# Kernel tuning notes

Measured on AMD Instinct MI355X. Metric: run time of the kernel, lower is better.

## Reference

```python
import jax, jax.numpy as jnp
import numpy as np

T, B, M, H = 2048, 16, 512, 256
R_MIN, R_MAX, MAX_PHASE = 0.0, 1.0, 6.28


def setup_inputs() -> dict:
    key = jax.random.key(0)
    ks = jax.random.split(key, 10)
    inputs = jax.random.normal(ks[0], (T, B, M), dtype=jnp.float32)
    h_re = jnp.zeros((B, H), dtype=jnp.float32)
    h_im = jnp.zeros((B, H), dtype=jnp.float32)
    # parameter inits matching the torch module (stable |lambda| < 1)
    u1 = jax.random.uniform(ks[1], (H,), dtype=jnp.float32)
    nu_log = jnp.log(-0.5 * jnp.log(u1 * (R_MAX**2 - R_MIN**2) + R_MIN**2))
    u2 = jax.random.uniform(ks[2], (H,), dtype=jnp.float32)
    theta_log = jnp.log(MAX_PHASE * u2)
    lam = jnp.exp(-jnp.exp(nu_log) + 1j * jnp.exp(theta_log))
    gamma_log = jnp.log(jnp.sqrt(1.0 - jnp.abs(lam) ** 2))
    B_re = jax.random.normal(ks[3], (H, M), dtype=jnp.float32) / np.sqrt(2 * M)
    B_im = jax.random.normal(ks[4], (H, M), dtype=jnp.float32) / np.sqrt(2 * M)
    C_re = jax.random.normal(ks[5], (M, H), dtype=jnp.float32) / np.sqrt(H)
    C_im = jax.random.normal(ks[6], (M, H), dtype=jnp.float32) / np.sqrt(H)
    D = jax.random.normal(ks[7], (M,), dtype=jnp.float32)
    return {"inputs": inputs, "h_re": h_re, "h_im": h_im,
            "nu_log": nu_log, "theta_log": theta_log, "gamma_log": gamma_log,
            "B_re": B_re, "B_im": B_im, "C_re": C_re, "C_im": C_im, "D": D}


def reference(inputs, h_re, h_im, nu_log, theta_log, gamma_log,
              B_re, B_im, C_re, C_im, D):
    # diag_lambda = exp(-exp(nu) + i exp(theta)), shape [H]
    lam = jnp.exp(jnp.complex64(-jnp.exp(nu_log) + 1j * jnp.exp(theta_log)))
    B_norm = (B_re + 1j * B_im) * jnp.exp(gamma_log)[:, None]  # [H, M] complex
    C = C_re + 1j * C_im                                        # [M, H] complex
    h0 = (h_re + 1j * h_im).astype(jnp.complex64)               # [B, H]
    Bu = inputs.astype(jnp.complex64) @ B_norm.T                # [T, B, H] precomputed input drive

    def step(h, xs):
        bu_t, x_t = xs
        h = h * lam + bu_t                                      # [B, H]
        y = jnp.real(h @ C.T) + D * x_t                         # [B, M]
        return h, y

    h_final, outputs = jax.lax.scan(step, h0, (Bu, inputs))
    return outputs, h_final
```

## Files before the change

### kernel.cpp

```cpp
#include <hip/hip_runtime.h>
#include <hip/hip_bf16.h>
#include <math.h>

#define T_DIM 2048
#define B_DIM 16
#define M_DIM 512
#define H_DIM 256
#define KC 512
#define K_DIM 512
#define CHUNK 64
#define NCHUNK 32
#define BK 32
#define NT (K_DIM / BK)

typedef unsigned short ushort_t;
typedef __attribute__((ext_vector_type(8))) short short8;
typedef __attribute__((ext_vector_type(8))) unsigned short ushort8;
typedef __attribute__((ext_vector_type(4))) float f32x4;

#define WS_LAM   0
#define WS_LAML  512
#define WS_CARRY 1024
#define WS_WB_BF 263168
#define WS_WC_BF 394240
#define WS_BU    525312

__device__ inline ushort_t f2bf(float f) {
    __hip_bfloat16 h = __float2bfloat16(f);
    return *reinterpret_cast<ushort_t*>(&h);
}
__device__ inline float bf2f(ushort_t u) {
    union { unsigned int i; float f; } v;
    v.i = ((unsigned int)u) << 16;
    return v.f;
}

__global__ void prep_lam(const float* __restrict__ nu_log,
                         const float* __restrict__ theta_log,
                         float* __restrict__ ws) {
    int h = threadIdx.x;
    float nu = expf(nu_log[h]);
    float th = expf(theta_log[h]);
    float r  = expf(-nu);
    ws[WS_LAM + h]        = r * cosf(th);
    ws[WS_LAM + 256 + h]  = r * sinf(th);
    float rL  = expf(-64.f * nu);
    float thL = 64.f * th;
    ws[WS_LAML + h]       = rL * cosf(thL);
    ws[WS_LAML + 256 + h] = rL * sinf(thL);
}

__global__ void prep_w(const float* __restrict__ B_re, const float* __restrict__ B_im,
                       const float* __restrict__ gamma_log,
                       const float* __restrict__ C_re, const float* __restrict__ C_im,
                       ushort_t* __restrict__ wb, ushort_t* __restrict__ wc) {
    int idx = blockIdx.x * blockDim.x + threadIdx.x;
    int e    = idx & 7;
    int slot = (idx >> 3) & 511;
    int row  = slot & 127;
    int ks   = slot >> 7;
    int t    = (idx >> 12) & 15;
    int blk  = idx >> 16;
    int j = blk * 128 + row;
    int k = t * 32 + ks * 8 + e;
    float v;
    if (j < 256) v = expf(gamma_log[j])       * B_re[j * 512 + k];
    else         v = expf(gamma_log[j - 256]) * B_im[(j - 256) * 512 + k];
    wb[idx] = f2bf(v);
    float w;
    if (k < 256) w =  C_re[j * 256 + k];
    else         w = -C_im[j * 256 + (k - 256)];
    wc[idx] = f2bf(w);
}

template <int A_BF16, int OUT_BF16>
__global__ __launch_bounds__(256) void gemm_mfma(
    const void* __restrict__ Aptr, const ushort_t* __restrict__ Wt,
    void* __restrict__ Cv, const float* __restrict__ Dv,
    const float* __restrict__ X) {
    __shared__ ushort_t Asl[2][4096];
    __shared__ ushort_t Bsl[2][4096];
    const int tid = threadIdx.x;
    const int bm = blockIdx.x << 7;
    const int bnb = blockIdx.y;
    const int bn = bnb << 7;
    const int lane = tid & 63;
    const int wid  = tid >> 6;
    const int wr  = (wid >> 1) << 6;
    const int wcc = (wid & 1) << 6;
    const int l16 = lane & 15;
    const int ksl = lane >> 4;

    const int c0 = tid, c1 = tid + 256;
    const int arow = tid >> 1;
    const int aks  = (tid & 1) << 1;
    const int as0  = (aks * 128 + arow) * 8;
    const int as1  = as0 + 1024;

    const float*    Af = (const float*)Aptr;
    const ushort_t* Ab = (const ushort_t*)Aptr;

    f32x4 acc[4][4] = {};
    float4 pva0, pva1, pvb0, pvb1;
    ushort8 pua0, pua1;

    auto stageB = [&](int t, int buf) {
        size_t base = ((size_t)(bnb * NT + t)) * 4096;
        __builtin_amdgcn_global_load_lds(
            (const __attribute__((address_space(1))) void*)(Wt + base + c0 * 8),
            (__attribute__((address_space(3))) void*)(&Bsl[buf][c0 * 8]), 16, 0, 0);
        __builtin_amdgcn_global_load_lds(
            (const __attribute__((address_space(1))) void*)(Wt + base + c1 * 8),
            (__attribute__((address_space(3))) void*)(&Bsl[buf][c1 * 8]), 16, 0, 0);
    };
    auto loadA = [&](int t) {
        if constexpr (A_BF16) {
            const ushort_t* p = Ab + (size_t)(bm + arow) * K_DIM + t * BK + aks * 8;
            pua0 = *(const ushort8*)(p);
            pua1 = *(const ushort8*)(p + 8);
        } else {
            const float* p = Af + (size_t)(bm + arow) * K_DIM + t * BK + aks * 8;
            pva0 = *(const float4*)(p);
            pva1 = *(const float4*)(p + 4);
            pvb0 = *(const float4*)(p + 8);
            pvb1 = *(const float4*)(p + 12);
        }
    };
    auto writeA = [&](int buf) {
        ushort8 u0, u1;
        if constexpr (A_BF16) {
            u0 = pua0; u1 = pua1;
        } else {
            u0[0] = f2bf(pva0.x); u0[1] = f2bf(pva0.y); u0[2] = f2bf(pva0.z); u0[3] = f2bf(pva0.w);
            u0[4] = f2bf(pva1.x); u0[5] = f2bf(pva1.y); u0[6] = f2bf(pva1.z); u0[7] = f2bf(pva1.w);
            u1[0] = f2bf(pvb0.x); u1[1] = f2bf(pvb0.y); u1[2] = f2bf(pvb0.z); u1[3] = f2bf(pvb0.w);
            u1[4] = f2bf(pvb1.x); u1[5] = f2bf(pvb1.y); u1[6] = f2bf(pvb1.z); u1[7] = f2bf(pvb1.w);
        }
        *(ushort8*)(&Asl[buf][as0]) = u0;
        *(ushort8*)(&Asl[buf][as1]) = u1;
    };

    stageB(0, 0);
    loadA(0);
    writeA(0);
    __syncthreads();

    int cur = 0;
#pragma unroll 2
    for (int t = 0; t < NT; ++t) {
        const int nxt = cur ^ 1;
        if (t + 1 < NT) { stageB(t + 1, nxt); loadA(t + 1); }
        short8 afr[4], bfr[4];
#pragma unroll
        for (int m = 0; m < 4; ++m)
            afr[m] = *(const short8*)(&Asl[cur][(ksl * 128 + wr + m * 16 + l16) * 8]);
#pragma unroll
        for (int n = 0; n < 4; ++n)
            bfr[n] = *(const short8*)(&Bsl[cur][(ksl * 128 + wcc + n * 16 + l16) * 8]);
#pragma unroll
        for (int m = 0; m < 4; ++m)
#pragma unroll
            for (int n = 0; n < 4; ++n)
                acc[m][n] = __builtin_amdgcn_mfma_f32_16x16x32_bf16(
                    afr[m], bfr[n], acc[m][n], 0, 0, 0);
        if (t + 1 < NT) writeA(nxt);
        __syncthreads();
        cur = nxt;
    }

    const int fr = (lane >> 4) << 2;
#pragma unroll
    for (int m = 0; m < 4; ++m) {
#pragma unroll
        for (int n = 0; n < 4; ++n) {
#pragma unroll
            for (int r = 0; r < 4; ++r) {
                int row = bm + wr + m * 16 + fr + r;
                int col = bn + wcc + n * 16 + l16;
                size_t o = (size_t)row * 512 + col;
                float v = acc[m][n][r];
                if constexpr (OUT_BF16) {
                    ((ushort_t*)Cv)[o] = f2bf(v);
                } else {
                    ((float*)Cv)[o] = v + Dv[col] * X[o];
                }
            }
        }
    }
}

__global__ __launch_bounds__(256) void scan_local(float* __restrict__ ws) {
    const int c = blockIdx.x >> 4;
    const int b = blockIdx.x & 15;
    const int h = threadIdx.x;
    const float lr = ws[WS_LAM + h], li = ws[WS_LAM + 256 + h];
    const ushort_t* Bu = (const ushort_t*)(ws + WS_BU);
    float hr = 0.f, hi = 0.f;
    const int t0 = c * CHUNK;
    for (int l = 0; l < CHUNK; ++l) {
        size_t idx = ((size_t)(t0 + l) * B_DIM + b) * KC + h;
        float br = bf2f(Bu[idx]), bi = bf2f(Bu[idx + 256]);
        float nr = fmaf(lr, hr, fmaf(-li, hi, br));
        float ni = fmaf(lr, hi, fmaf(li, hr, bi));
        hr = nr; hi = ni;
    }
    size_t cidx = ((size_t)(c * B_DIM + b)) * KC + h;
    ws[WS_CARRY + cidx]       = hr;
    ws[WS_CARRY + cidx + 256] = hi;
}

__global__ __launch_bounds__(256) void scan_carry(float* __restrict__ ws,
        const float* __restrict__ h_re, const float* __restrict__ h_im,
        float* __restrict__ out, int out_size) {
    const int b = blockIdx.x;
    const int h = threadIdx.x;
    const float Lr = ws[WS_LAML + h], Li = ws[WS_LAML + 256 + h];
    float cr = h_re[b * H_DIM + h], ci = h_im[b * H_DIM + h];
    for (int c = 0; c < NCHUNK; ++c) {
        size_t cidx = ((size_t)(c * B_DIM + b)) * KC + h;
        float sr = ws[WS_CARRY + cidx], si = ws[WS_CARRY + cidx + 256];
        ws[WS_CARRY + cidx]       = cr;
        ws[WS_CARRY + cidx + 256] = ci;
        float nr = fmaf(Lr, cr, fmaf(-Li, ci, sr));
        float ni = fmaf(Lr, ci, fmaf(Li, cr, si));
        cr = nr; ci = ni;
    }
    const size_t base = (size_t)T_DIM * B_DIM * M_DIM;
    const size_t idx  = (size_t)b * H_DIM + h;
    size_t ore = base + idx;
    size_t oim = base + (size_t)B_DIM * H_DIM + idx;
    if (ore < (size_t)out_size) out[ore] = cr;
    if (oim < (size_t)out_size) out[oim] = ci;
}

__global__ __launch_bounds__(256) void scan_apply(float* __restrict__ ws) {
    const int c = blockIdx.x >> 4;
    const int b = blockIdx.x & 15;
    const int h = threadIdx.x;
    const float lr = ws[WS_LAM + h], li = ws[WS_LAM + 256 + h];
    ushort_t* Bu = (ushort_t*)(ws + WS_BU);
    size_t cidx = ((size_t)(c * B_DIM + b)) * KC + h;
    float hr = ws[WS_CARRY + cidx], hi = ws[WS_CARRY + cidx + 256];
    const int t0 = c * CHUNK;
    for (int l = 0; l < CHUNK; ++l) {
        size_t idx = ((size_t)(t0 + l) * B_DIM + b) * KC + h;
        float br = bf2f(Bu[idx]), bi = bf2f(Bu[idx + 256]);
        float nr = fmaf(lr, hr, fmaf(-li, hi, br));
        float ni = fmaf(lr, hi, fmaf(li, hr, bi));
        hr = nr; hi = ni;
        Bu[idx]       = f2bf(hr);
        Bu[idx + 256] = f2bf(hi);
    }
}

extern "C" void kernel_launch(void* const* d_in, const int* in_sizes, int n_in,
                              void* d_out, int out_size, void* d_ws, size_t ws_size,
                              hipStream_t stream) {
    const float* inputs    = (const float*)d_in[0];
    const float* h_re      = (const float*)d_in[1];
    const float* h_im      = (const float*)d_in[2];
    const float* nu_log    = (const float*)d_in[3];
    const float* theta_log = (const float*)d_in[4];
    const float* gamma_log = (const float*)d_in[5];
    const float* B_re      = (const float*)d_in[6];
    const float* B_im      = (const float*)d_in[7];
    const float* C_re      = (const float*)d_in[8];
    const float* C_im      = (const float*)d_in[9];
    const float* Dv        = (const float*)d_in[10];
    float* out = (float*)d_out;
    float* ws  = (float*)d_ws;
    ushort_t* wb = (ushort_t*)(ws + WS_WB_BF);
    ushort_t* wc = (ushort_t*)(ws + WS_WC_BF);
    ushort_t* bu = (ushort_t*)(ws + WS_BU);

    prep_lam<<<1, 256, 0, stream>>>(nu_log, theta_log, ws);
    prep_w<<<1024, 256, 0, stream>>>(B_re, B_im, gamma_log, C_re, C_im, wb, wc);

    gemm_mfma<0, 1><<<dim3(256, 4), 256, 0, stream>>>(inputs, wb, (void*)bu,
                                                      nullptr, nullptr);

    scan_local<<<NCHUNK * B_DIM, 256, 0, stream>>>(ws);
    scan_carry<<<B_DIM, 256, 0, stream>>>(ws, h_re, h_im, out, out_size);
    scan_apply<<<NCHUNK * B_DIM, 256, 0, stream>>>(ws);

    gemm_mfma<1, 0><<<dim3(256, 4), 256, 0, stream>>>(bu, wc, (void*)out,
                                                      Dv, inputs);
}
```

Measured before the change: 115.9 us.

## Write scan output in pre-tiled layout and stage both GEMM operands via LDS DMA

scan_apply now writes the hidden states into a separate buffer arranged in the tiled layout the second GEMM reads. That GEMM can then load its A operand with global_load_lds direct-to-LDS copies instead of register loads followed by LDS stores. The prep_lam kernel is removed, and each scan kernel recomputes lambda in-line, which saves a launch at the cost of some redundant transcendental math. MFMA sections are wrapped in s_setprio, and the unroll pragma on the k-loop is dropped. The scattered 2-byte stores in scan_apply may coalesce less well than before.

```diff
diff --git a/kernel.cpp b/kernel.cpp
--- a/kernel.cpp
+++ b/kernel.cpp
@@ -11,19 +11,18 @@
 #define CHUNK 64
 #define NCHUNK 32
 #define BK 32
-#define NT (K_DIM / BK)
+#define NTILE 16
 
 typedef unsigned short ushort_t;
 typedef __attribute__((ext_vector_type(8))) short short8;
 typedef __attribute__((ext_vector_type(8))) unsigned short ushort8;
 typedef __attribute__((ext_vector_type(4))) float f32x4;
 
-#define WS_LAM   0
-#define WS_LAML  512
-#define WS_CARRY 1024
-#define WS_WB_BF 263168
-#define WS_WC_BF 394240
-#define WS_BU    525312
+#define WS_CARRY 0
+#define WS_WB_BF 262144
+#define WS_WC_BF 393216
+#define WS_BU    524288
+#define WS_HT    8912896
 
 __device__ inline ushort_t f2bf(float f) {
     __hip_bfloat16 h = __float2bfloat16(f);
@@ -33,21 +32,6 @@
     union { unsigned int i; float f; } v;
     v.i = ((unsigned int)u) << 16;
     return v.f;
-}
-
-__global__ void prep_lam(const float* __restrict__ nu_log,
-                         const float* __restrict__ theta_log,
-                         float* __restrict__ ws) {
-    int h = threadIdx.x;
-    float nu = expf(nu_log[h]);
-    float th = expf(theta_log[h]);
-    float r  = expf(-nu);
-    ws[WS_LAM + h]        = r * cosf(th);
-    ws[WS_LAM + 256 + h]  = r * sinf(th);
-    float rL  = expf(-64.f * nu);
-    float thL = 64.f * th;
-    ws[WS_LAML + h]       = rL * cosf(thL);
-    ws[WS_LAML + 256 + h] = rL * sinf(thL);
 }
 
 __global__ void prep_w(const float* __restrict__ B_re, const float* __restrict__ B_im,
@@ -73,7 +57,7 @@
     wc[idx] = f2bf(w);
 }
 
-template <int A_BF16, int OUT_BF16>
+template <int A_TILED, int OUT_BF16>
 __global__ __launch_bounds__(256) void gemm_mfma(
     const void* __restrict__ Aptr, const ushort_t* __restrict__ Wt,
     void* __restrict__ Cv, const float* __restrict__ Dv,
@@ -81,16 +65,13 @@
     __shared__ ushort_t Asl[2][4096];
     __shared__ ushort_t Bsl[2][4096];
     const int tid = threadIdx.x;
-    const int bm = blockIdx.x << 7;
-    const int bnb = blockIdx.y;
-    const int bn = bnb << 7;
-    const int lane = tid & 63;
-    const int wid  = tid >> 6;
+    const int rb = blockIdx.x;
+    const int nb = blockIdx.y;
+    const int bm = rb << 7, bn = nb << 7;
+    const int lane = tid & 63, wid = tid >> 6;
     const int wr  = (wid >> 1) << 6;
     const int wcc = (wid & 1) << 6;
-    const int l16 = lane & 15;
-    const int ksl = lane >> 4;
-
+    const int l16 = lane & 15, ksl = lane >> 4;
     const int c0 = tid, c1 = tid + 256;
     const int arow = tid >> 1;
     const int aks  = (tid & 1) << 1;
@@ -98,27 +79,13 @@
     const int as1  = as0 + 1024;
 
     const float*    Af = (const float*)Aptr;
-    const ushort_t* Ab = (const ushort_t*)Aptr;
+    const ushort_t* At = (const ushort_t*)Aptr;
 
     f32x4 acc[4][4] = {};
     float4 pva0, pva1, pvb0, pvb1;
-    ushort8 pua0, pua1;
-
-    auto stageB = [&](int t, int buf) {
-        size_t base = ((size_t)(bnb * NT + t)) * 4096;
-        __builtin_amdgcn_global_load_lds(
-            (const __attribute__((address_space(1))) void*)(Wt + base + c0 * 8),
-            (__attribute__((address_space(3))) void*)(&Bsl[buf][c0 * 8]), 16, 0, 0);
-        __builtin_amdgcn_global_load_lds(
-            (const __attribute__((address_space(1))) void*)(Wt + base + c1 * 8),
-            (__attribute__((address_space(3))) void*)(&Bsl[buf][c1 * 8]), 16, 0, 0);
-    };
+
     auto loadA = [&](int t) {
-        if constexpr (A_BF16) {
-            const ushort_t* p = Ab + (size_t)(bm + arow) * K_DIM + t * BK + aks * 8;
-            pua0 = *(const ushort8*)(p);
-            pua1 = *(const ushort8*)(p + 8);
-        } else {
+        if constexpr (!A_TILED) {
             const float* p = Af + (size_t)(bm + arow) * K_DIM + t * BK + aks * 8;
             pva0 = *(const float4*)(p);
             pva1 = *(const float4*)(p + 4);
@@ -126,30 +93,45 @@
             pvb1 = *(const float4*)(p + 12);
         }
     };
+    auto stage = [&](int t, int buf) {
+        if constexpr (A_TILED) {
+            size_t ab = ((size_t)(rb * NTILE + t)) * 4096;
+            __builtin_amdgcn_global_load_lds(
+                (const __attribute__((address_space(1))) void*)(At + ab + c0 * 8),
+                (__attribute__((address_space(3))) void*)(&Asl[buf][c0 * 8]), 16, 0, 0);
+            __builtin_amdgcn_global_load_lds(
+                (const __attribute__((address_space(1))) void*)(At + ab + c1 * 8),
+                (__attribute__((address_space(3))) void*)(&Asl[buf][c1 * 8]), 16, 0, 0);
+        }
+        size_t bb = ((size_t)(nb * NTILE + t)) * 4096;
+        __builtin_amdgcn_global_load_lds(
+            (const __attribute__((address_space(1))) void*)(Wt + bb + c0 * 8),
+            (__attribute__((address_space(3))) void*)(&Bsl[buf][c0 * 8]), 16, 0, 0);
+        __builtin_amdgcn_global_load_lds(
+            (const __attribute__((address_space(1))) void*)(Wt + bb + c1 * 8),
+            (__attribute__((address_space(3))) void*)(&Bsl[buf][c1 * 8]), 16, 0, 0);
+    };
     auto writeA = [&](int buf) {
-        ushort8 u0, u1;
-        if constexpr (A_BF16) {
-            u0 = pua0; u1 = pua1;
-        } else {
+        if constexpr (!A_TILED) {
+            ushort8 u0, u1;
             u0[0] = f2bf(pva0.x); u0[1] = f2bf(pva0.y); u0[2] = f2bf(pva0.z); u0[3] = f2bf(pva0.w);
             u0[4] = f2bf(pva1.x); u0[5] = f2bf(pva1.y); u0[6] = f2bf(pva1.z); u0[7] = f2bf(pva1.w);
             u1[0] = f2bf(pvb0.x); u1[1] = f2bf(pvb0.y); u1[2] = f2bf(pvb0.z); u1[3] = f2bf(pvb0.w);
             u1[4] = f2bf(pvb1.x); u1[5] = f2bf(pvb1.y); u1[6] = f2bf(pvb1.z); u1[7] = f2bf(pvb1.w);
-        }
-        *(ushort8*)(&Asl[buf][as0]) = u0;
-        *(ushort8*)(&Asl[buf][as1]) = u1;
+            *(ushort8*)(&Asl[buf][as0]) = u0;
+            *(ushort8*)(&Asl[buf][as1]) = u1;
+        }
     };
 
-    stageB(0, 0);
     loadA(0);
+    stage(0, 0);
     writeA(0);
     __syncthreads();
 
     int cur = 0;
-#pragma unroll 2
-    for (int t = 0; t < NT; ++t) {
+    for (int t = 0; t < NTILE; ++t) {
         const int nxt = cur ^ 1;
-        if (t + 1 < NT) { stageB(t + 1, nxt); loadA(t + 1); }
+        if (t + 1 < NTILE) { loadA(t + 1); stage(t + 1, nxt); }
         short8 afr[4], bfr[4];
 #pragma unroll
         for (int m = 0; m < 4; ++m)
@@ -157,13 +139,15 @@
 #pragma unroll
         for (int n = 0; n < 4; ++n)
             bfr[n] = *(const short8*)(&Bsl[cur][(ksl * 128 + wcc + n * 16 + l16) * 8]);
+        __builtin_amdgcn_s_setprio(1);
 #pragma unroll
         for (int m = 0; m < 4; ++m)
 #pragma unroll
             for (int n = 0; n < 4; ++n)
                 acc[m][n] = __builtin_amdgcn_mfma_f32_16x16x32_bf16(
                     afr[m], bfr[n], acc[m][n], 0, 0, 0);
-        if (t + 1 < NT) writeA(nxt);
+        __builtin_amdgcn_s_setprio(0);
+        if (t + 1 < NTILE) writeA(nxt);
         __syncthreads();
         cur = nxt;
     }
@@ -189,11 +173,15 @@
     }
 }
 
-__global__ __launch_bounds__(256) void scan_local(float* __restrict__ ws) {
+__global__ __launch_bounds__(256) void scan_local(const float* __restrict__ nu_log,
+        const float* __restrict__ theta_log, float* __restrict__ ws) {
     const int c = blockIdx.x >> 4;
     const int b = blockIdx.x & 15;
     const int h = threadIdx.x;
-    const float lr = ws[WS_LAM + h], li = ws[WS_LAM + 256 + h];
+    const float nu = expf(nu_log[h]);
+    const float th = expf(theta_log[h]);
+    const float r  = expf(-nu);
+    const float lr = r * cosf(th), li = r * sinf(th);
     const ushort_t* Bu = (const ushort_t*)(ws + WS_BU);
     float hr = 0.f, hi = 0.f;
     const int t0 = c * CHUNK;
@@ -209,12 +197,17 @@
     ws[WS_CARRY + cidx + 256] = hi;
 }
 
-__global__ __launch_bounds__(256) void scan_carry(float* __restrict__ ws,
+__global__ __launch_bounds__(256) void scan_carry(const float* __restrict__ nu_log,
+        const float* __restrict__ theta_log, float* __restrict__ ws,
         const float* __restrict__ h_re, const float* __restrict__ h_im,
         float* __restrict__ out, int out_size) {
     const int b = blockIdx.x;
     const int h = threadIdx.x;
-    const float Lr = ws[WS_LAML + h], Li = ws[WS_LAML + 256 + h];
+    const float nu = expf(nu_log[h]);
+    const float th = expf(theta_log[h]);
+    const float rL  = expf(-64.f * nu);
+    const float thL = 64.f * th;
+    const float Lr = rL * cosf(thL), Li = rL * sinf(thL);
     float cr = h_re[b * H_DIM + h], ci = h_im[b * H_DIM + h];
     for (int c = 0; c < NCHUNK; ++c) {
         size_t cidx = ((size_t)(c * B_DIM + b)) * KC + h;
@@ -233,23 +226,35 @@
     if (oim < (size_t)out_size) out[oim] = ci;
 }
 
-__global__ __launch_bounds__(256) void scan_apply(float* __restrict__ ws) {
+__global__ __launch_bounds__(256) void scan_apply(const float* __restrict__ nu_log,
+        const float* __restrict__ theta_log, float* __restrict__ ws) {
     const int c = blockIdx.x >> 4;
     const int b = blockIdx.x & 15;
     const int h = threadIdx.x;
-    const float lr = ws[WS_LAM + h], li = ws[WS_LAM + 256 + h];
-    ushort_t* Bu = (ushort_t*)(ws + WS_BU);
+    const float nu = expf(nu_log[h]);
+    const float th = expf(theta_log[h]);
+    const float rr = expf(-nu);
+    const float lr = rr * cosf(th), li = rr * sinf(th);
+    const ushort_t* Bu = (const ushort_t*)(ws + WS_BU);
+    ushort_t* Ht = (ushort_t*)(ws + WS_HT);
     size_t cidx = ((size_t)(c * B_DIM + b)) * KC + h;
     float hr = ws[WS_CARRY + cidx], hi = ws[WS_CARRY + cidx + 256];
+    const int t_re = h >> 5;
+    const int ks_e = (h >> 3) & 3;
+    const int e_   = h & 7;
     const int t0 = c * CHUNK;
     for (int l = 0; l < CHUNK; ++l) {
-        size_t idx = ((size_t)(t0 + l) * B_DIM + b) * KC + h;
+        int n = (t0 + l) * B_DIM + b;
+        size_t idx = (size_t)n * KC + h;
         float br = bf2f(Bu[idx]), bi = bf2f(Bu[idx + 256]);
         float nr = fmaf(lr, hr, fmaf(-li, hi, br));
         float ni = fmaf(lr, hi, fmaf(li, hr, bi));
         hr = nr; hi = ni;
-        Bu[idx]       = f2bf(hr);
-        Bu[idx + 256] = f2bf(hi);
+        int rbk = n >> 7, rr_ = n & 127;
+        size_t ire = (((size_t)(rbk * NTILE + t_re)) * 512 + ks_e * 128 + rr_) * 8 + e_;
+        size_t iim = (((size_t)(rbk * NTILE + t_re + 8)) * 512 + ks_e * 128 + rr_) * 8 + e_;
+        Ht[ire] = f2bf(hr);
+        Ht[iim] = f2bf(hi);
     }
 }
 
@@ -272,17 +277,18 @@
     ushort_t* wb = (ushort_t*)(ws + WS_WB_BF);
     ushort_t* wc = (ushort_t*)(ws + WS_WC_BF);
     ushort_t* bu = (ushort_t*)(ws + WS_BU);
-
-    prep_lam<<<1, 256, 0, stream>>>(nu_log, theta_log, ws);
+    ushort_t* ht = (ushort_t*)(ws + WS_HT);
+
     prep_w<<<1024, 256, 0, stream>>>(B_re, B_im, gamma_log, C_re, C_im, wb, wc);
 
     gemm_mfma<0, 1><<<dim3(256, 4), 256, 0, stream>>>(inputs, wb, (void*)bu,
                                                       nullptr, nullptr);
 
-    scan_local<<<NCHUNK * B_DIM, 256, 0, stream>>>(ws);
-    scan_carry<<<B_DIM, 256, 0, stream>>>(ws, h_re, h_im, out, out_size);
-    scan_apply<<<NCHUNK * B_DIM, 256, 0, stream>>>(ws);
-
-    gemm_mfma<1, 0><<<dim3(256, 4), 256, 0, stream>>>(bu, wc, (void*)out,
+    scan_local<<<NCHUNK * B_DIM, 256, 0, stream>>>(nu_log, theta_log, ws);
+    scan_carry<<<B_DIM, 256, 0, stream>>>(nu_log, theta_log, ws, h_re, h_im,
+                                          out, out_size);
+    scan_apply<<<NCHUNK * B_DIM, 256, 0, stream>>>(nu_log, theta_log, ws);
+
+    gemm_mfma<1, 0><<<dim3(256, 4), 256, 0, stream>>>(ht, wc, (void*)out,
                                                       Dv, inputs);
 }
```

Result: slower. 156.1 us (+34.8%).
